# Kernel optimization log

Measured on AMD Instinct MI355X. Metric: run time of the kernel, lower is better.

Reference implementation:

```python
import jax, jax.numpy as jnp
import numpy as np

N = 50000      # nodes
E = 800000     # edges (avg degree 16)
F_IN = 128
H = 128
C = 64


def _lin(k, fan_in, fan_out):
    bound = 1.0 / np.sqrt(fan_in)
    kw, kb = jax.random.split(k)
    W = jax.random.uniform(kw, (fan_in, fan_out), jnp.float32, -bound, bound)
    b = jax.random.uniform(kb, (fan_out,), jnp.float32, -bound, bound)
    return W, b


def setup_inputs() -> dict:
    key = jax.random.key(0)
    ks = jax.random.split(key, 8)
    W1, b1 = _lin(ks[3], F_IN, H)
    W2, b2 = _lin(ks[4], H, H)
    W3, b3 = _lin(ks[5], H, H)
    Wr, br = _lin(ks[6], F_IN, H)
    Wo, bo = _lin(ks[7], H, C)
    return {
        "x": jax.random.normal(ks[0], (N, F_IN), jnp.float32),
        "src": jax.random.randint(ks[1], (E,), 0, N, jnp.int32),
        "dst": jax.random.randint(ks[2], (E,), 0, N, jnp.int32),
        "W1": W1, "b1": b1,
        "W2": W2, "b2": b2,
        "W3": W3, "b3": b3,
        "Wr": Wr, "br": br,
        "Wo": Wo, "bo": bo,
    }


def _degree_norms(src, dst, n):
    ones = jnp.ones(src.shape[0], jnp.float32)
    deg_out = jax.ops.segment_sum(ones, src, num_segments=n)
    deg_in = jax.ops.segment_sum(ones, dst, num_segments=n)
    # DGL norm='both': clamp zero-degree to 1 to avoid inf
    d_src = jnp.where(deg_out > 0, deg_out, 1.0) ** -0.5
    d_dst = jnp.where(deg_in > 0, deg_in, 1.0) ** -0.5
    return d_src, d_dst


def _graph_conv(x, W, b, src, dst, d_src, d_dst, n):
    # h = D_dst^{-1/2} A D_src^{-1/2} (x W) + b
    h = (x * d_src[:, None]) @ W              # [N, out]
    agg = jax.ops.segment_sum(h[src], dst, num_segments=n)  # SpMM via gather/scatter
    return agg * d_dst[:, None] + b


def reference(x, src, dst, W1, b1, W2, b2, W3, b3, Wr, br, Wo, bo):
    n = x.shape[0]
    d_src, d_dst = _degree_norms(src, dst, n)
    res = x @ Wr + br
    out = jax.nn.relu(_graph_conv(x, W1, b1, src, dst, d_src, d_dst, n))
    out = jax.nn.relu(_graph_conv(out, W2, b2, src, dst, d_src, d_dst, n))
    out = _graph_conv(out, W3, b3, src, dst, d_src, d_dst, n)
    out = jax.nn.relu(out + res)
    return out @ Wo + bo
```

## Files before the change

### kernel.cpp

```cpp
#include <hip/hip_runtime.h>
#include <cstdint>
#include <cstddef>

#define FD 128
#define CO 64
#define NB 256
#define NBINS 256

typedef short bf16x8 __attribute__((ext_vector_type(8)));
typedef float f32x4 __attribute__((ext_vector_type(4)));
typedef unsigned int uint32;
typedef unsigned char uint8;

__device__ __forceinline__ unsigned short f2bf(float f) {
  unsigned u = __float_as_uint(f);
  unsigned r = u + 0x7fffu + ((u >> 16) & 1u);
  return (unsigned short)(r >> 16);
}
__device__ __forceinline__ float bf2f(unsigned short b) {
  return __uint_as_float((unsigned)b << 16);
}


__global__ __launch_bounds__(256) void k_hist(const int* __restrict__ src,
                                              const int* __restrict__ dst,
                                              int* __restrict__ histD,
                                              int* __restrict__ histS,
                                              int E, int chunk) {
  __shared__ int hd[NBINS], hs[NBINS];
  int tid = threadIdx.x, blk = blockIdx.x;
  hd[tid] = 0;
  hs[tid] = 0;
  __syncthreads();
  int beg = blk * chunk;
  int end = min(E, beg + chunk);
  for (int e = beg + tid; e < end; e += 256) {
    atomicAdd(&hd[dst[e] >> 8], 1);
    atomicAdd(&hs[src[e] >> 8], 1);
  }
  __syncthreads();
  histD[tid * NB + blk] = hd[tid];
  histS[tid * NB + blk] = hs[tid];
}


__global__ __launch_bounds__(256) void k_ssum(int* __restrict__ a,
                                              int* __restrict__ b,
                                              int* __restrict__ bsums) {
  const int* p = blockIdx.y ? b : a;
  __shared__ int red[256];
  int tid = threadIdx.x;
  red[tid] = p[blockIdx.x * 256 + tid];
  __syncthreads();
  for (int o = 128; o > 0; o >>= 1) {
    if (tid < o) red[tid] += red[tid + o];
    __syncthreads();
  }
  if (tid == 0) bsums[blockIdx.y * 256 + blockIdx.x] = red[0];
}

__global__ __launch_bounds__(256) void k_sscan(int* __restrict__ bsums) {
  __shared__ int s[256];
  int tid = threadIdx.x;
  for (int r = 0; r < 2; r++) {
    int v = bsums[r * 256 + tid];
    s[tid] = v;
    __syncthreads();
    for (int o = 1; o < 256; o <<= 1) {
      int t = (tid >= o) ? s[tid - o] : 0;
      __syncthreads();
      s[tid] += t;
      __syncthreads();
    }
    bsums[r * 256 + tid] = s[tid] - v;
    __syncthreads();
  }
}

__global__ __launch_bounds__(256) void k_sapply(int* __restrict__ a,
                                                int* __restrict__ b,
                                                const int* __restrict__ bsums) {
  int* p = blockIdx.y ? b : a;
  int boff = bsums[blockIdx.y * 256 + blockIdx.x];
  __shared__ int s[256];
  int tid = threadIdx.x;
  int i = blockIdx.x * 256 + tid;
  int v = p[i];
  s[tid] = v;
  __syncthreads();
  for (int o = 1; o < 256; o <<= 1) {
    int t = (tid >= o) ? s[tid - o] : 0;
    __syncthreads();
    s[tid] += t;
    __syncthreads();
  }
  p[i] = boff + s[tid] - v;
}

__global__ __launch_bounds__(256) void k_scatter(const int* __restrict__ src,
                                                 const int* __restrict__ dst,
                                                 const int* __restrict__ offD,
                                                 const int* __restrict__ offS,
                                                 uint32* __restrict__ pk,
                                                 uint8* __restrict__ srcS8,
                                                 int E, int chunk) {
  __shared__ int runD[NBINS], runS[NBINS];
  int tid = threadIdx.x, blk = blockIdx.x;
  runD[tid] = offD[tid * NB + blk];
  runS[tid] = offS[tid * NB + blk];
  __syncthreads();
  int beg = blk * chunk;
  int end = min(E, beg + chunk);
  for (int e = beg + tid; e < end; e += 256) {
    int s = src[e], d = dst[e];
    int p = atomicAdd(&runD[d >> 8], 1);
    pk[p] = ((uint32)s << 8) | (uint32)(d & 255);
    int q = atomicAdd(&runS[s >> 8], 1);
    srcS8[q] = (uint8)(s & 255);
  }
}

__global__ __launch_bounds__(256) void k_bucket_dst(const uint32* __restrict__ pk,
                                                    const int* __restrict__ offD,
                                                    int* __restrict__ esrc,
                                                    int* __restrict__ row_ptr,
                                                    float* __restrict__ d_dst,
                                                    int N, int E) {
  __shared__ int cnt[NBINS], run[NBINS];
  int tid = threadIdx.x, bin = blockIdx.x;
  int start = offD[bin * NB];
  int end = (bin == NBINS - 1) ? E : offD[(bin + 1) * NB];
  cnt[tid] = 0;
  __syncthreads();
  for (int p = start + tid; p < end; p += 256) atomicAdd(&cnt[pk[p] & 255], 1);
  __syncthreads();
  int v = cnt[tid];
  run[tid] = v;
  __syncthreads();
  for (int o = 1; o < 256; o <<= 1) {
    int t = (tid >= o) ? run[tid - o] : 0;
    __syncthreads();
    run[tid] += t;
    __syncthreads();
  }
  int excl = run[tid] - v;
  int node = bin * 256 + tid;
  if (node < N) {
    row_ptr[node] = start + excl;
    d_dst[node] = rsqrtf((float)(v > 0 ? v : 1));
  }
  __syncthreads();
  run[tid] = start + excl;
  __syncthreads();
  for (int p = start + tid; p < end; p += 256) {
    uint32 v2 = pk[p];
    int slot = atomicAdd(&run[v2 & 255], 1);
    esrc[slot] = (int)(v2 >> 8);
  }
  if (bin == 0 && tid == 0) row_ptr[N] = E;
}

__global__ __launch_bounds__(256) void k_bucket_src(const uint8* __restrict__ srcS8,
                                                    const int* __restrict__ offS,
                                                    float* __restrict__ d_src,
                                                    int N, int E) {
  __shared__ int cnt[NBINS];
  int tid = threadIdx.x, bin = blockIdx.x;
  int start = offS[bin * NB];
  int end = (bin == NBINS - 1) ? E : offS[(bin + 1) * NB];
  cnt[tid] = 0;
  __syncthreads();
  for (int p = start + tid; p < end; p += 256) atomicAdd(&cnt[srcS8[p]], 1);
  __syncthreads();
  int node = bin * 256 + tid;
  if (node < N) {
    int v = cnt[tid];
    d_src[node] = rsqrtf((float)(v > 0 ? v : 1));
  }
}


__global__ __launch_bounds__(256) void k_wsplit(const float* __restrict__ W1,
                                                const float* __restrict__ W2,
                                                const float* __restrict__ W3,
                                                const float* __restrict__ Wr,
                                                const float* __restrict__ Wo,
                                                bf16x8* __restrict__ Whg,
                                                bf16x8* __restrict__ Wlg) {
  int idx = blockIdx.x * 256 + threadIdx.x;
  if (idx >= 9216) return;
  int region = idx >> 11;
  if (idx >= 8192) region = 4;
  const float* W = (region == 0) ? W1 : (region == 1) ? W2 : (region == 2) ? W3
                   : (region == 3) ? Wr : Wo;
  int cols = (region < 4) ? FD : CO;
  int local = idx - region * 2048;
  int kc = local / cols, col = local - kc * cols;
  bf16x8 h, l;
#pragma unroll
  for (int j = 0; j < 8; j++) {
    float v = W[(size_t)(kc * 8 + j) * cols + col];
    unsigned short hb = f2bf(v);
    h[j] = (short)hb;
    l[j] = (short)f2bf(v - bf2f(hb));
  }
  Whg[idx] = h;
  Wlg[idx] = l;
}


__global__ __launch_bounds__(256) void k_gemm_dual(const float* __restrict__ x,
                                                   const bf16x8* __restrict__ Wh1,
                                                   const bf16x8* __restrict__ Wl1,
                                                   const float* __restrict__ d_src,
                                                   const bf16x8* __restrict__ Whr,
                                                   const bf16x8* __restrict__ Wlr,
                                                   const float* __restrict__ br,
                                                   unsigned short* __restrict__ out1,
                                                   unsigned short* __restrict__ out2,
                                                   int N) {
  __shared__ bf16x8 Ah[1024];
  int tid = threadIdx.x;
  int rowBase = blockIdx.x * 64;

#pragma unroll
  for (int t = 0; t < 4; t++) {
    int p = t * 256 + tid;
    int kc = p >> 6, row = p & 63;
    int gr = rowBase + row;
    bf16x8 h = {0, 0, 0, 0, 0, 0, 0, 0};
    if (gr < N) {
      const float4* A4 = (const float4*)(x + (size_t)gr * FD + kc * 8);
      float4 u = A4[0];
      float4 v = A4[1];
      float vals[8] = {u.x, u.y, u.z, u.w, v.x, v.y, v.z, v.w};
#pragma unroll
      for (int j = 0; j < 8; j++) h[j] = (short)f2bf(vals[j]);
    }
    Ah[kc * 64 + row] = h;
  }
  __syncthreads();

  int wv = tid >> 6, lane = tid & 63;
  int wr = (wv >> 1) * 32;
  int wc = (wv & 1) * 64;
  int lhi = lane >> 4, llo = lane & 15;

#pragma unroll
  for (int pass = 0; pass < 2; pass++) {
    const bf16x8* Wh = pass ? Whr : Wh1;
    const bf16x8* Wl = pass ? Wlr : Wl1;
    f32x4 acc[2][4] = {};
#pragma unroll
    for (int ks = 0; ks < 4; ks++) {
      int kcg = ks * 4 + lhi;
      int abase = kcg * 64 + wr + llo;
      bf16x8 a0 = Ah[abase];
      bf16x8 a1 = Ah[abase + 16];
      int bbase = kcg * FD + wc + llo;
#pragma unroll
      for (int nf = 0; nf < 4; nf++) {
        bf16x8 bh = Wh[bbase + nf * 16];
        bf16x8 bl = Wl[bbase + nf * 16];
        acc[0][nf] = __builtin_amdgcn_mfma_f32_16x16x32_bf16(a0, bh, acc[0][nf], 0, 0, 0);
        acc[1][nf] = __builtin_amdgcn_mfma_f32_16x16x32_bf16(a1, bh, acc[1][nf], 0, 0, 0);
        acc[0][nf] = __builtin_amdgcn_mfma_f32_16x16x32_bf16(a0, bl, acc[0][nf], 0, 0, 0);
        acc[1][nf] = __builtin_amdgcn_mfma_f32_16x16x32_bf16(a1, bl, acc[1][nf], 0, 0, 0);
      }
    }
#pragma unroll
    for (int nf = 0; nf < 4; nf++) {
      int col = wc + nf * 16 + llo;
      float bv = pass ? br[col] : 0.f;
#pragma unroll
      for (int mf = 0; mf < 2; mf++) {
#pragma unroll
        for (int r = 0; r < 4; r++) {
          int row = rowBase + wr + mf * 16 + lhi * 4 + r;
          if (row < N) {
            float v = acc[mf][nf][r];
            if (pass == 0) v *= d_src[row];
            else v += bv;
            unsigned short* o = pass ? out2 : out1;
            o[(size_t)row * FD + col] = f2bf(v);
          }
        }
      }
    }
  }
}


template <int NCW, bool RES, bool NEXTSCALE, bool BIASOUT, bool OUTBF16>
__global__ __launch_bounds__(512) void k_aggemm(const unsigned short* __restrict__ h,
                                                const int* __restrict__ row_ptr,
                                                const int* __restrict__ esrc,
                                                const float* __restrict__ d_dst,
                                                const float* __restrict__ bias_in,
                                                const float* __restrict__ d_src,
                                                const unsigned short* __restrict__ res,
                                                const bf16x8* __restrict__ Wh,
                                                const bf16x8* __restrict__ Wl,
                                                const float* __restrict__ bias_out,
                                                void* __restrict__ outv, int N) {
  constexpr int NF = NCW / 64;
  __shared__ bf16x8 Alds[1024];
  int tid = threadIdx.x;
  int wv = tid >> 6, lane = tid & 63;
  int rowBase = blockIdx.x * 64;
  int sub = lane >> 4, sl = lane & 15;
  const uint4* h16 = (const uint4*)h;

  float4 bA = ((const float4*)bias_in)[sl * 2];
  float4 bB = ((const float4*)bias_in)[sl * 2 + 1];
  float bia[8] = {bA.x, bA.y, bA.z, bA.w, bB.x, bB.y, bB.z, bB.w};

  for (int rq = 0; rq < 2; rq++) {
    int r = wv * 8 + rq * 4 + sub;
    int gr = rowBase + r;
    float a[8] = {0.f, 0.f, 0.f, 0.f, 0.f, 0.f, 0.f, 0.f};
    float val[8];
    if (gr < N) {
      int beg = row_ptr[gr], end = row_ptr[gr + 1];
      int e = beg;
      for (; e + 8 <= end; e += 8) {
        int s[8];
#pragma unroll
        for (int j = 0; j < 8; j++) s[j] = esrc[e + j];
        uint4 v[8];
#pragma unroll
        for (int j = 0; j < 8; j++) v[j] = h16[(size_t)s[j] * 16 + sl];
#pragma unroll
        for (int j = 0; j < 8; j++) {
          a[0] += bf2f((unsigned short)(v[j].x & 0xffff));
          a[1] += bf2f((unsigned short)(v[j].x >> 16));
          a[2] += bf2f((unsigned short)(v[j].y & 0xffff));
          a[3] += bf2f((unsigned short)(v[j].y >> 16));
          a[4] += bf2f((unsigned short)(v[j].z & 0xffff));
          a[5] += bf2f((unsigned short)(v[j].z >> 16));
          a[6] += bf2f((unsigned short)(v[j].w & 0xffff));
          a[7] += bf2f((unsigned short)(v[j].w >> 16));
        }
      }
      for (; e < end; e++) {
        uint4 v = h16[(size_t)esrc[e] * 16 + sl];
        a[0] += bf2f((unsigned short)(v.x & 0xffff));
        a[1] += bf2f((unsigned short)(v.x >> 16));
        a[2] += bf2f((unsigned short)(v.y & 0xffff));
        a[3] += bf2f((unsigned short)(v.y >> 16));
        a[4] += bf2f((unsigned short)(v.z & 0xffff));
        a[5] += bf2f((unsigned short)(v.z >> 16));
        a[6] += bf2f((unsigned short)(v.w & 0xffff));
        a[7] += bf2f((unsigned short)(v.w >> 16));
      }
      float d = d_dst[gr];
#pragma unroll
      for (int j = 0; j < 8; j++) val[j] = a[j] * d + bia[j];
      if (RES) {
        uint4 rv = ((const uint4*)res)[(size_t)gr * 16 + sl];
        val[0] += bf2f((unsigned short)(rv.x & 0xffff));
        val[1] += bf2f((unsigned short)(rv.x >> 16));
        val[2] += bf2f((unsigned short)(rv.y & 0xffff));
        val[3] += bf2f((unsigned short)(rv.y >> 16));
        val[4] += bf2f((unsigned short)(rv.z & 0xffff));
        val[5] += bf2f((unsigned short)(rv.z >> 16));
        val[6] += bf2f((unsigned short)(rv.w & 0xffff));
        val[7] += bf2f((unsigned short)(rv.w >> 16));
      }
#pragma unroll
      for (int j = 0; j < 8; j++) val[j] = fmaxf(val[j], 0.f);
      if (NEXTSCALE) {
        float sc = d_src[gr];
#pragma unroll
        for (int j = 0; j < 8; j++) val[j] *= sc;
      }
    } else {
#pragma unroll
      for (int j = 0; j < 8; j++) val[j] = 0.f;
    }
    bf16x8 o;
#pragma unroll
    for (int j = 0; j < 8; j++) o[j] = (short)f2bf(val[j]);
    Alds[r * 16 + (sl ^ (r & 7))] = o;
  }
  __syncthreads();

  int wr = (wv >> 2) * 32;
  int wc = (wv & 3) * (NCW / 4);
  int lhi = lane >> 4, llo = lane & 15;
  f32x4 acc[2][NF] = {};

#pragma unroll
  for (int ks = 0; ks < 4; ks++) {
    int kcg = ks * 4 + lhi;
    int row0 = wr + llo;
    int row1 = wr + 16 + llo;
    bf16x8 a0 = Alds[row0 * 16 + (kcg ^ (row0 & 7))];
    bf16x8 a1 = Alds[row1 * 16 + (kcg ^ (row1 & 7))];
    int bbase = kcg * NCW + wc + llo;
#pragma unroll
    for (int nf = 0; nf < NF; nf++) {
      bf16x8 bh = Wh[bbase + nf * 16];
      bf16x8 bl = Wl[bbase + nf * 16];
      acc[0][nf] = __builtin_amdgcn_mfma_f32_16x16x32_bf16(a0, bh, acc[0][nf], 0, 0, 0);
      acc[1][nf] = __builtin_amdgcn_mfma_f32_16x16x32_bf16(a1, bh, acc[1][nf], 0, 0, 0);
      acc[0][nf] = __builtin_amdgcn_mfma_f32_16x16x32_bf16(a0, bl, acc[0][nf], 0, 0, 0);
      acc[1][nf] = __builtin_amdgcn_mfma_f32_16x16x32_bf16(a1, bl, acc[1][nf], 0, 0, 0);
    }
  }

#pragma unroll
  for (int nf = 0; nf < NF; nf++) {
    int col = wc + nf * 16 + llo;
    float bv = BIASOUT ? bias_out[col] : 0.f;
#pragma unroll
    for (int mf = 0; mf < 2; mf++) {
#pragma unroll
      for (int r = 0; r < 4; r++) {
        int row = rowBase + wr + mf * 16 + lhi * 4 + r;
        if (row < N) {
          float v = acc[mf][nf][r] + bv;
          if (OUTBF16)
            ((unsigned short*)outv)[(size_t)row * NCW + col] = f2bf(v);
          else
            ((float*)outv)[(size_t)row * NCW + col] = v;
        }
      }
    }
  }
}


extern "C" void kernel_launch(void* const* d_in, const int* in_sizes, int n_in,
                              void* d_out, int out_size, void* d_ws, size_t ws_size,
                              hipStream_t stream) {
  (void)n_in; (void)out_size; (void)ws_size;
  const float* x  = (const float*)d_in[0];
  const int*   src = (const int*)d_in[1];
  const int*   dst = (const int*)d_in[2];
  const float* W1 = (const float*)d_in[3];
  const float* b1 = (const float*)d_in[4];
  const float* W2 = (const float*)d_in[5];
  const float* b2 = (const float*)d_in[6];
  const float* W3 = (const float*)d_in[7];
  const float* b3 = (const float*)d_in[8];
  const float* Wr = (const float*)d_in[9];
  const float* br = (const float*)d_in[10];
  const float* Wo = (const float*)d_in[11];
  const float* bo = (const float*)d_in[12];
  float* out = (float*)d_out;

  const int N = in_sizes[0] / FD;
  const int E = in_sizes[1];

  char* ws = (char*)d_ws;
  size_t off = 0;
  auto alloc = [&](size_t bytes) -> void* {
    void* p = ws + off;
    off += (bytes + 255) & ~size_t(255);
    return p;
  };
  int* histD   = (int*)alloc((size_t)NBINS * NB * 4);
  int* histS   = (int*)alloc((size_t)NBINS * NB * 4);
  int* bsums   = (int*)alloc(2 * 256 * 4);
  uint32* pk   = (uint32*)alloc((size_t)E * 4);
  uint8* srcS8 = (uint8*)alloc((size_t)E);
  int* esrc    = (int*)alloc((size_t)E * 4);
  int* row_ptr = (int*)alloc((size_t)(N + 1) * 4);
  float* d_src = (float*)alloc((size_t)N * 4);
  float* d_dst = (float*)alloc((size_t)N * 4);
  bf16x8* Whg  = (bf16x8*)alloc(9216 * 16);
  bf16x8* Wlg  = (bf16x8*)alloc(9216 * 16);
  unsigned short* tb0  = (unsigned short*)alloc((size_t)N * FD * 2);
  unsigned short* tb1  = (unsigned short*)alloc((size_t)N * FD * 2);
  unsigned short* resb = (unsigned short*)alloc((size_t)N * FD * 2);

  int chunk = (E + NB - 1) / NB;
  dim3 gScan(256, 2);

  k_wsplit<<<36, 256, 0, stream>>>(W1, W2, W3, Wr, Wo, Whg, Wlg);
  k_hist<<<NB, 256, 0, stream>>>(src, dst, histD, histS, E, chunk);
  k_ssum<<<gScan, 256, 0, stream>>>(histD, histS, bsums);
  k_sscan<<<1, 256, 0, stream>>>(bsums);
  k_sapply<<<gScan, 256, 0, stream>>>(histD, histS, bsums);
  k_scatter<<<NB, 256, 0, stream>>>(src, dst, histD, histS, pk, srcS8, E, chunk);
  k_bucket_dst<<<NBINS, 256, 0, stream>>>(pk, histD, esrc, row_ptr, d_dst, N, E);
  k_bucket_src<<<NBINS, 256, 0, stream>>>(srcS8, histS, d_src, N, E);

  int gG = (N + 63) / 64;

  const bf16x8* Wh1 = Whg;
  const bf16x8* Wh2 = Whg + 2048;
  const bf16x8* Wh3 = Whg + 4096;
  const bf16x8* Whr = Whg + 6144;
  const bf16x8* Who = Whg + 8192;
  const bf16x8* Wl1 = Wlg;
  const bf16x8* Wl2 = Wlg + 2048;
  const bf16x8* Wl3 = Wlg + 4096;
  const bf16x8* Wlr = Wlg + 6144;
  const bf16x8* Wlo = Wlg + 8192;

  k_gemm_dual<<<gG, 256, 0, stream>>>(x, Wh1, Wl1, d_src, Whr, Wlr, br, tb0, resb, N);
  k_aggemm<FD, false, true, false, true><<<gG, 512, 0, stream>>>(
      tb0, row_ptr, esrc, d_dst, b1, d_src, nullptr, Wh2, Wl2, nullptr, tb1, N);
  k_aggemm<FD, false, true, false, true><<<gG, 512, 0, stream>>>(
      tb1, row_ptr, esrc, d_dst, b2, d_src, nullptr, Wh3, Wl3, nullptr, tb0, N);
  k_aggemm<CO, true, false, true, false><<<gG, 512, 0, stream>>>(
      tb0, row_ptr, esrc, d_dst, b3, nullptr, resb, Who, Wlo, bo, out, N);
}
```

Before: 210.0 us.

## Split fused aggregate-GEMM into column-partitioned aggregation and separate GEMM kernels

Replaces the fused aggregation+MFMA kernel with two kernels per layer. The first is a gather aggregation whose grid is split four ways over column quarters, so each thread handles 8 columns for one node. The second is a standalone split-bf16 GEMM that reads the aggregated bf16 intermediate. The aim is more parallelism and better latency hiding for the gather, at the cost of writing and re-reading an extra N×128 bf16 buffer and three more kernel launches. Each edge-index read is also repeated across the four column blocks.

```diff
diff --git a/kernel.cpp b/kernel.cpp
--- a/kernel.cpp
+++ b/kernel.cpp
@@ -11,13 +11,14 @@
 typedef float f32x4 __attribute__((ext_vector_type(4)));
 typedef unsigned int uint32;
 typedef unsigned char uint8;
-
-__device__ __forceinline__ unsigned short f2bf(float f) {
+typedef unsigned short ushort;
+
+__device__ __forceinline__ ushort f2bf(float f) {
   unsigned u = __float_as_uint(f);
   unsigned r = u + 0x7fffu + ((u >> 16) & 1u);
-  return (unsigned short)(r >> 16);
-}
-__device__ __forceinline__ float bf2f(unsigned short b) {
+  return (ushort)(r >> 16);
+}
+__device__ __forceinline__ float bf2f(ushort b) {
   return __uint_as_float((unsigned)b << 16);
 }
 
@@ -42,7 +43,6 @@
   histD[tid * NB + blk] = hd[tid];
   histS[tid * NB + blk] = hs[tid];
 }
-
 
 __global__ __launch_bounds__(256) void k_ssum(int* __restrict__ a,
                                               int* __restrict__ b,
@@ -200,7 +200,7 @@
 #pragma unroll
   for (int j = 0; j < 8; j++) {
     float v = W[(size_t)(kc * 8 + j) * cols + col];
-    unsigned short hb = f2bf(v);
+    ushort hb = f2bf(v);
     h[j] = (short)hb;
     l[j] = (short)f2bf(v - bf2f(hb));
   }
@@ -216,8 +216,8 @@
                                                    const bf16x8* __restrict__ Whr,
                                                    const bf16x8* __restrict__ Wlr,
                                                    const float* __restrict__ br,
-                                                   unsigned short* __restrict__ out1,
-                                                   unsigned short* __restrict__ out2,
+                                                   ushort* __restrict__ out1,
+                                                   ushort* __restrict__ out2,
                                                    int N) {
   __shared__ bf16x8 Ah[1024];
   int tid = threadIdx.x;
@@ -281,7 +281,7 @@
             float v = acc[mf][nf][r];
             if (pass == 0) v *= d_src[row];
             else v += bv;
-            unsigned short* o = pass ? out2 : out1;
+            ushort* o = pass ? out2 : out1;
             o[(size_t)row * FD + col] = f2bf(v);
           }
         }
@@ -291,112 +291,130 @@
 }
 
 
-template <int NCW, bool RES, bool NEXTSCALE, bool BIASOUT, bool OUTBF16>
-__global__ __launch_bounds__(512) void k_aggemm(const unsigned short* __restrict__ h,
-                                                const int* __restrict__ row_ptr,
-                                                const int* __restrict__ esrc,
-                                                const float* __restrict__ d_dst,
-                                                const float* __restrict__ bias_in,
-                                                const float* __restrict__ d_src,
-                                                const unsigned short* __restrict__ res,
-                                                const bf16x8* __restrict__ Wh,
-                                                const bf16x8* __restrict__ Wl,
-                                                const float* __restrict__ bias_out,
-                                                void* __restrict__ outv, int N) {
-  constexpr int NF = NCW / 64;
-  __shared__ bf16x8 Alds[1024];
+template <bool RES, bool NEXTSCALE>
+__global__ __launch_bounds__(256) void k_agg4(const ushort* __restrict__ h,
+                                              const int* __restrict__ row_ptr,
+                                              const int* __restrict__ esrc,
+                                              const float* __restrict__ d_dst,
+                                              const float* __restrict__ bias_in,
+                                              const float* __restrict__ d_src,
+                                              const ushort* __restrict__ res,
+                                              ushort* __restrict__ out,
+                                              int N, int nodeBlocks) {
+  int blk = blockIdx.x;
+  int q = blk / nodeBlocks;
+  int nb = blk - q * nodeBlocks;
   int tid = threadIdx.x;
+  int sub = tid >> 2, sl = tid & 3;
+  int node = nb * 64 + sub;
+  if (node >= N) return;
+  int colSlot = q * 4 + sl;
+  const uint4* h16 = (const uint4*)h;
+
+  float4 bA = ((const float4*)bias_in)[q * 8 + sl * 2];
+  float4 bB = ((const float4*)bias_in)[q * 8 + sl * 2 + 1];
+  float bia[8] = {bA.x, bA.y, bA.z, bA.w, bB.x, bB.y, bB.z, bB.w};
+
+  int beg = row_ptr[node], end = row_ptr[node + 1];
+  float a[8] = {0.f, 0.f, 0.f, 0.f, 0.f, 0.f, 0.f, 0.f};
+  int e = beg;
+  for (; e + 8 <= end; e += 8) {
+    int s[8];
+#pragma unroll
+    for (int j = 0; j < 8; j++) s[j] = esrc[e + j];
+    uint4 v[8];
+#pragma unroll
+    for (int j = 0; j < 8; j++) v[j] = h16[(size_t)s[j] * 16 + colSlot];
+#pragma unroll
+    for (int j = 0; j < 8; j++) {
+      a[0] += bf2f((ushort)(v[j].x & 0xffff));
+      a[1] += bf2f((ushort)(v[j].x >> 16));
+      a[2] += bf2f((ushort)(v[j].y & 0xffff));
+      a[3] += bf2f((ushort)(v[j].y >> 16));
+      a[4] += bf2f((ushort)(v[j].z & 0xffff));
+      a[5] += bf2f((ushort)(v[j].z >> 16));
+      a[6] += bf2f((ushort)(v[j].w & 0xffff));
+      a[7] += bf2f((ushort)(v[j].w >> 16));
+    }
+  }
+  for (; e < end; e++) {
+    uint4 v = h16[(size_t)esrc[e] * 16 + colSlot];
+    a[0] += bf2f((ushort)(v.x & 0xffff));
+    a[1] += bf2f((ushort)(v.x >> 16));
+    a[2] += bf2f((ushort)(v.y & 0xffff));
+    a[3] += bf2f((ushort)(v.y >> 16));
+    a[4] += bf2f((ushort)(v.z & 0xffff));
+    a[5] += bf2f((ushort)(v.z >> 16));
+    a[6] += bf2f((ushort)(v.w & 0xffff));
+    a[7] += bf2f((ushort)(v.w >> 16));
+  }
+
+  float d = d_dst[node];
+  float val[8];
+#pragma unroll
+  for (int j = 0; j < 8; j++) val[j] = a[j] * d + bia[j];
+  if (RES) {
+    uint4 rv = ((const uint4*)res)[(size_t)node * 16 + colSlot];
+    val[0] += bf2f((ushort)(rv.x & 0xffff));
+    val[1] += bf2f((ushort)(rv.x >> 16));
+    val[2] += bf2f((ushort)(rv.y & 0xffff));
+    val[3] += bf2f((ushort)(rv.y >> 16));
+    val[4] += bf2f((ushort)(rv.z & 0xffff));
+    val[5] += bf2f((ushort)(rv.z >> 16));
+    val[6] += bf2f((ushort)(rv.w & 0xffff));
+    val[7] += bf2f((ushort)(rv.w >> 16));
+  }
+#pragma unroll
+  for (int j = 0; j < 8; j++) val[j] = fmaxf(val[j], 0.f);
+  if (NEXTSCALE) {
+    float sc = d_src[node];
+#pragma unroll
+    for (int j = 0; j < 8; j++) val[j] *= sc;
+  }
+  uint32 w0 = (uint32)f2bf(val[0]) | ((uint32)f2bf(val[1]) << 16);
+  uint32 w1 = (uint32)f2bf(val[2]) | ((uint32)f2bf(val[3]) << 16);
+  uint32 w2 = (uint32)f2bf(val[4]) | ((uint32)f2bf(val[5]) << 16);
+  uint32 w3 = (uint32)f2bf(val[6]) | ((uint32)f2bf(val[7]) << 16);
+  uint4 o;
+  o.x = w0; o.y = w1; o.z = w2; o.w = w3;
+  ((uint4*)out)[(size_t)node * 16 + colSlot] = o;
+}
+
+
+template <int NCW, bool BIAS, bool OUTBF16>
+__global__ __launch_bounds__(256) void k_gemmB(const ushort* __restrict__ A,
+                                               const bf16x8* __restrict__ Wh,
+                                               const bf16x8* __restrict__ Wl,
+                                               const float* __restrict__ bias,
+                                               void* __restrict__ outv, int N) {
+  constexpr int NF = NCW / 32;
+  __shared__ bf16x8 Ah[1024];
+  int tid = threadIdx.x;
+  int rowBase = blockIdx.x * 64;
+
+#pragma unroll
+  for (int t = 0; t < 4; t++) {
+    int p = t * 256 + tid;
+    int kc = p >> 6, row = p & 63;
+    int gr = rowBase + row;
+    bf16x8 h = {0, 0, 0, 0, 0, 0, 0, 0};
+    if (gr < N) h = *(const bf16x8*)(A + (size_t)gr * FD + kc * 8);
+    Ah[kc * 64 + row] = h;
+  }
+  __syncthreads();
+
   int wv = tid >> 6, lane = tid & 63;
-  int rowBase = blockIdx.x * 64;
-  int sub = lane >> 4, sl = lane & 15;
-  const uint4* h16 = (const uint4*)h;
-
-  float4 bA = ((const float4*)bias_in)[sl * 2];
-  float4 bB = ((const float4*)bias_in)[sl * 2 + 1];
-  float bia[8] = {bA.x, bA.y, bA.z, bA.w, bB.x, bB.y, bB.z, bB.w};
-
-  for (int rq = 0; rq < 2; rq++) {
-    int r = wv * 8 + rq * 4 + sub;
-    int gr = rowBase + r;
-    float a[8] = {0.f, 0.f, 0.f, 0.f, 0.f, 0.f, 0.f, 0.f};
-    float val[8];
-    if (gr < N) {
-      int beg = row_ptr[gr], end = row_ptr[gr + 1];
-      int e = beg;
-      for (; e + 8 <= end; e += 8) {
-        int s[8];
-#pragma unroll
-        for (int j = 0; j < 8; j++) s[j] = esrc[e + j];
-        uint4 v[8];
-#pragma unroll
-        for (int j = 0; j < 8; j++) v[j] = h16[(size_t)s[j] * 16 + sl];
-#pragma unroll
-        for (int j = 0; j < 8; j++) {
-          a[0] += bf2f((unsigned short)(v[j].x & 0xffff));
-          a[1] += bf2f((unsigned short)(v[j].x >> 16));
-          a[2] += bf2f((unsigned short)(v[j].y & 0xffff));
-          a[3] += bf2f((unsigned short)(v[j].y >> 16));
-          a[4] += bf2f((unsigned short)(v[j].z & 0xffff));
-          a[5] += bf2f((unsigned short)(v[j].z >> 16));
-          a[6] += bf2f((unsigned short)(v[j].w & 0xffff));
-          a[7] += bf2f((unsigned short)(v[j].w >> 16));
-        }
-      }
-      for (; e < end; e++) {
-        uint4 v = h16[(size_t)esrc[e] * 16 + sl];
-        a[0] += bf2f((unsigned short)(v.x & 0xffff));
-        a[1] += bf2f((unsigned short)(v.x >> 16));
-        a[2] += bf2f((unsigned short)(v.y & 0xffff));
-        a[3] += bf2f((unsigned short)(v.y >> 16));
-        a[4] += bf2f((unsigned short)(v.z & 0xffff));
-        a[5] += bf2f((unsigned short)(v.z >> 16));
-        a[6] += bf2f((unsigned short)(v.w & 0xffff));
-        a[7] += bf2f((unsigned short)(v.w >> 16));
-      }
-      float d = d_dst[gr];
-#pragma unroll
-      for (int j = 0; j < 8; j++) val[j] = a[j] * d + bia[j];
-      if (RES) {
-        uint4 rv = ((const uint4*)res)[(size_t)gr * 16 + sl];
-        val[0] += bf2f((unsigned short)(rv.x & 0xffff));
-        val[1] += bf2f((unsigned short)(rv.x >> 16));
-        val[2] += bf2f((unsigned short)(rv.y & 0xffff));
-        val[3] += bf2f((unsigned short)(rv.y >> 16));
-        val[4] += bf2f((unsigned short)(rv.z & 0xffff));
-        val[5] += bf2f((unsigned short)(rv.z >> 16));
-        val[6] += bf2f((unsigned short)(rv.w & 0xffff));
-        val[7] += bf2f((unsigned short)(rv.w >> 16));
-      }
-#pragma unroll
-      for (int j = 0; j < 8; j++) val[j] = fmaxf(val[j], 0.f);
-      if (NEXTSCALE) {
-        float sc = d_src[gr];
-#pragma unroll
-        for (int j = 0; j < 8; j++) val[j] *= sc;
-      }
-    } else {
-#pragma unroll
-      for (int j = 0; j < 8; j++) val[j] = 0.f;
-    }
-    bf16x8 o;
-#pragma unroll
-    for (int j = 0; j < 8; j++) o[j] = (short)f2bf(val[j]);
-    Alds[r * 16 + (sl ^ (r & 7))] = o;
-  }
-  __syncthreads();
-
-  int wr = (wv >> 2) * 32;
-  int wc = (wv & 3) * (NCW / 4);
+  int wr = (wv >> 1) * 32;
+  int wc = (wv & 1) * (NCW / 2);
   int lhi = lane >> 4, llo = lane & 15;
   f32x4 acc[2][NF] = {};
 
 #pragma unroll
   for (int ks = 0; ks < 4; ks++) {
     int kcg = ks * 4 + lhi;
-    int row0 = wr + llo;
-    int row1 = wr + 16 + llo;
-    bf16x8 a0 = Alds[row0 * 16 + (kcg ^ (row0 & 7))];
-    bf16x8 a1 = Alds[row1 * 16 + (kcg ^ (row1 & 7))];
+    int abase = kcg * 64 + wr + llo;
+    bf16x8 a0 = Ah[abase];
+    bf16x8 a1 = Ah[abase + 16];
     int bbase = kcg * NCW + wc + llo;
 #pragma unroll
     for (int nf = 0; nf < NF; nf++) {
@@ -412,7 +430,7 @@
 #pragma unroll
   for (int nf = 0; nf < NF; nf++) {
     int col = wc + nf * 16 + llo;
-    float bv = BIASOUT ? bias_out[col] : 0.f;
+    float bv = BIAS ? bias[col] : 0.f;
 #pragma unroll
     for (int mf = 0; mf < 2; mf++) {
 #pragma unroll
@@ -421,7 +439,7 @@
         if (row < N) {
           float v = acc[mf][nf][r] + bv;
           if (OUTBF16)
-            ((unsigned short*)outv)[(size_t)row * NCW + col] = f2bf(v);
+            ((ushort*)outv)[(size_t)row * NCW + col] = f2bf(v);
           else
             ((float*)outv)[(size_t)row * NCW + col] = v;
         }
@@ -471,9 +489,10 @@
   float* d_dst = (float*)alloc((size_t)N * 4);
   bf16x8* Whg  = (bf16x8*)alloc(9216 * 16);
   bf16x8* Wlg  = (bf16x8*)alloc(9216 * 16);
-  unsigned short* tb0  = (unsigned short*)alloc((size_t)N * FD * 2);
-  unsigned short* tb1  = (unsigned short*)alloc((size_t)N * FD * 2);
-  unsigned short* resb = (unsigned short*)alloc((size_t)N * FD * 2);
+  ushort* tb0  = (ushort*)alloc((size_t)N * FD * 2);
+  ushort* tb1  = (ushort*)alloc((size_t)N * FD * 2);
+  ushort* tba  = (ushort*)alloc((size_t)N * FD * 2);
+  ushort* resb = (ushort*)alloc((size_t)N * FD * 2);
 
   int chunk = (E + NB - 1) / NB;
   dim3 gScan(256, 2);
@@ -488,6 +507,8 @@
   k_bucket_src<<<NBINS, 256, 0, stream>>>(srcS8, histS, d_src, N, E);
 
   int gG = (N + 63) / 64;
+  int nodeBlocks = (N + 63) / 64;
+  int gA = nodeBlocks * 4;
 
   const bf16x8* Wh1 = Whg;
   const bf16x8* Wh2 = Whg + 2048;
@@ -501,10 +522,13 @@
   const bf16x8* Wlo = Wlg + 8192;
 
   k_gemm_dual<<<gG, 256, 0, stream>>>(x, Wh1, Wl1, d_src, Whr, Wlr, br, tb0, resb, N);
-  k_aggemm<FD, false, true, false, true><<<gG, 512, 0, stream>>>(
-      tb0, row_ptr, esrc, d_dst, b1, d_src, nullptr, Wh2, Wl2, nullptr, tb1, N);
-  k_aggemm<FD, false, true, false, true><<<gG, 512, 0, stream>>>(
-      tb1, row_ptr, esrc, d_dst, b2, d_src, nullptr, Wh3, Wl3, nullptr, tb0, N);
-  k_aggemm<CO, true, false, true, false><<<gG, 512, 0, stream>>>(
-      tb0, row_ptr, esrc, d_dst, b3, nullptr, resb, Who, Wlo, bo, out, N);
-}
+  k_agg4<false, true><<<gA, 256, 0, stream>>>(tb0, row_ptr, esrc, d_dst, b1, d_src,
+                                              nullptr, tba, N, nodeBlocks);
+  k_gemmB<FD, false, true><<<gG, 256, 0, stream>>>(tba, Wh2, Wl2, nullptr, tb1, N);
+  k_agg4<false, true><<<gA, 256, 0, stream>>>(tb1, row_ptr, esrc, d_dst, b2, d_src,
+                                              nullptr, tba, N, nodeBlocks);
+  k_gemmB<FD, false, true><<<gG, 256, 0, stream>>>(tba, Wh3, Wl3, nullptr, tb0, N);
+  k_agg4<true, false><<<gA, 256, 0, stream>>>(tb0, row_ptr, esrc, d_dst, b3, nullptr,
+                                              resb, tba, N, nodeBlocks);
+  k_gemmB<CO, true, false><<<gG, 256, 0, stream>>>(tba, Who, Wlo, bo, out, N);
+}
```

Result: slower. 253.4 us (+20.7%).

## Use 16-bit edge indices and 1024-thread aggregation blocks with deeper gather unroll

Applied to the files above, without the earlier changes.

Edge source indices in the CSR are stored as 16-bit values instead of 32-bit, halving index traffic in the gather loops. The aggregate+GEMM kernel now runs 1024 threads per block, so each 16-lane group handles one row instead of two and each wave does a 16-row MFMA tile. The neighbor gather unrolls by 16 with a masked tail instead of 8 plus a scalar tail. The aim is more outstanding memory requests for the latency-bound gather. The 16-bit indices only work while the node count stays below 65536, and the larger blocks may lower occupancy flexibility.

```diff
diff --git a/kernel.cpp b/kernel.cpp
--- a/kernel.cpp
+++ b/kernel.cpp
@@ -11,13 +11,14 @@
 typedef float f32x4 __attribute__((ext_vector_type(4)));
 typedef unsigned int uint32;
 typedef unsigned char uint8;
-
-__device__ __forceinline__ unsigned short f2bf(float f) {
+typedef unsigned short ushort;
+
+__device__ __forceinline__ ushort f2bf(float f) {
   unsigned u = __float_as_uint(f);
   unsigned r = u + 0x7fffu + ((u >> 16) & 1u);
-  return (unsigned short)(r >> 16);
-}
-__device__ __forceinline__ float bf2f(unsigned short b) {
+  return (ushort)(r >> 16);
+}
+__device__ __forceinline__ float bf2f(ushort b) {
   return __uint_as_float((unsigned)b << 16);
 }
 
@@ -42,7 +43,6 @@
   histD[tid * NB + blk] = hd[tid];
   histS[tid * NB + blk] = hs[tid];
 }
-
 
 __global__ __launch_bounds__(256) void k_ssum(int* __restrict__ a,
                                               int* __restrict__ b,
@@ -122,7 +122,7 @@
 
 __global__ __launch_bounds__(256) void k_bucket_dst(const uint32* __restrict__ pk,
                                                     const int* __restrict__ offD,
-                                                    int* __restrict__ esrc,
+                                                    ushort* __restrict__ esrc,
                                                     int* __restrict__ row_ptr,
                                                     float* __restrict__ d_dst,
                                                     int N, int E) {
@@ -155,7 +155,7 @@
   for (int p = start + tid; p < end; p += 256) {
     uint32 v2 = pk[p];
     int slot = atomicAdd(&run[v2 & 255], 1);
-    esrc[slot] = (int)(v2 >> 8);
+    esrc[slot] = (ushort)(v2 >> 8);
   }
   if (bin == 0 && tid == 0) row_ptr[N] = E;
 }
@@ -200,7 +200,7 @@
 #pragma unroll
   for (int j = 0; j < 8; j++) {
     float v = W[(size_t)(kc * 8 + j) * cols + col];
-    unsigned short hb = f2bf(v);
+    ushort hb = f2bf(v);
     h[j] = (short)hb;
     l[j] = (short)f2bf(v - bf2f(hb));
   }
@@ -216,8 +216,8 @@
                                                    const bf16x8* __restrict__ Whr,
                                                    const bf16x8* __restrict__ Wlr,
                                                    const float* __restrict__ br,
-                                                   unsigned short* __restrict__ out1,
-                                                   unsigned short* __restrict__ out2,
+                                                   ushort* __restrict__ out1,
+                                                   ushort* __restrict__ out2,
                                                    int N) {
   __shared__ bf16x8 Ah[1024];
   int tid = threadIdx.x;
@@ -281,7 +281,7 @@
             float v = acc[mf][nf][r];
             if (pass == 0) v *= d_src[row];
             else v += bv;
-            unsigned short* o = pass ? out2 : out1;
+            ushort* o = pass ? out2 : out1;
             o[(size_t)row * FD + col] = f2bf(v);
           }
         }
@@ -292,120 +292,126 @@
 
 
 template <int NCW, bool RES, bool NEXTSCALE, bool BIASOUT, bool OUTBF16>
-__global__ __launch_bounds__(512) void k_aggemm(const unsigned short* __restrict__ h,
-                                                const int* __restrict__ row_ptr,
-                                                const int* __restrict__ esrc,
-                                                const float* __restrict__ d_dst,
-                                                const float* __restrict__ bias_in,
-                                                const float* __restrict__ d_src,
-                                                const unsigned short* __restrict__ res,
-                                                const bf16x8* __restrict__ Wh,
-                                                const bf16x8* __restrict__ Wl,
-                                                const float* __restrict__ bias_out,
-                                                void* __restrict__ outv, int N) {
+__global__ __launch_bounds__(1024) void k_aggemm(const ushort* __restrict__ h,
+                                                 const int* __restrict__ row_ptr,
+                                                 const ushort* __restrict__ esrc,
+                                                 const float* __restrict__ d_dst,
+                                                 const float* __restrict__ bias_in,
+                                                 const float* __restrict__ d_src,
+                                                 const ushort* __restrict__ res,
+                                                 const bf16x8* __restrict__ Wh,
+                                                 const bf16x8* __restrict__ Wl,
+                                                 const float* __restrict__ bias_out,
+                                                 void* __restrict__ outv, int N) {
   constexpr int NF = NCW / 64;
   __shared__ bf16x8 Alds[1024];
   int tid = threadIdx.x;
   int wv = tid >> 6, lane = tid & 63;
   int rowBase = blockIdx.x * 64;
   int sub = lane >> 4, sl = lane & 15;
+  int r = wv * 4 + sub;
+  int gr = rowBase + r;
   const uint4* h16 = (const uint4*)h;
 
   float4 bA = ((const float4*)bias_in)[sl * 2];
   float4 bB = ((const float4*)bias_in)[sl * 2 + 1];
   float bia[8] = {bA.x, bA.y, bA.z, bA.w, bB.x, bB.y, bB.z, bB.w};
 
-  for (int rq = 0; rq < 2; rq++) {
-    int r = wv * 8 + rq * 4 + sub;
-    int gr = rowBase + r;
+  float val[8];
+#pragma unroll
+  for (int j = 0; j < 8; j++) val[j] = 0.f;
+
+  if (gr < N) {
+    int beg = row_ptr[gr], end = row_ptr[gr + 1];
     float a[8] = {0.f, 0.f, 0.f, 0.f, 0.f, 0.f, 0.f, 0.f};
-    float val[8];
-    if (gr < N) {
-      int beg = row_ptr[gr], end = row_ptr[gr + 1];
-      int e = beg;
-      for (; e + 8 <= end; e += 8) {
-        int s[8];
-#pragma unroll
-        for (int j = 0; j < 8; j++) s[j] = esrc[e + j];
-        uint4 v[8];
-#pragma unroll
-        for (int j = 0; j < 8; j++) v[j] = h16[(size_t)s[j] * 16 + sl];
-#pragma unroll
-        for (int j = 0; j < 8; j++) {
-          a[0] += bf2f((unsigned short)(v[j].x & 0xffff));
-          a[1] += bf2f((unsigned short)(v[j].x >> 16));
-          a[2] += bf2f((unsigned short)(v[j].y & 0xffff));
-          a[3] += bf2f((unsigned short)(v[j].y >> 16));
-          a[4] += bf2f((unsigned short)(v[j].z & 0xffff));
-          a[5] += bf2f((unsigned short)(v[j].z >> 16));
-          a[6] += bf2f((unsigned short)(v[j].w & 0xffff));
-          a[7] += bf2f((unsigned short)(v[j].w >> 16));
+    int e = beg;
+    for (; e + 16 <= end; e += 16) {
+      int s[16];
+#pragma unroll
+      for (int j = 0; j < 16; j++) s[j] = esrc[e + j];
+      uint4 v[16];
+#pragma unroll
+      for (int j = 0; j < 16; j++) v[j] = h16[(size_t)s[j] * 16 + sl];
+#pragma unroll
+      for (int j = 0; j < 16; j++) {
+        a[0] += bf2f((ushort)(v[j].x & 0xffff));
+        a[1] += bf2f((ushort)(v[j].x >> 16));
+        a[2] += bf2f((ushort)(v[j].y & 0xffff));
+        a[3] += bf2f((ushort)(v[j].y >> 16));
+        a[4] += bf2f((ushort)(v[j].z & 0xffff));
+        a[5] += bf2f((ushort)(v[j].z >> 16));
+        a[6] += bf2f((ushort)(v[j].w & 0xffff));
+        a[7] += bf2f((ushort)(v[j].w >> 16));
+      }
+    }
+    if (e < end) {
+      int cnt = end - e;
+      int s[16];
+#pragma unroll
+      for (int j = 0; j < 16; j++) s[j] = (j < cnt) ? (int)esrc[e + j] : 0;
+      uint4 v[16];
+#pragma unroll
+      for (int j = 0; j < 16; j++)
+        if (j < cnt) v[j] = h16[(size_t)s[j] * 16 + sl];
+#pragma unroll
+      for (int j = 0; j < 16; j++) {
+        if (j < cnt) {
+          a[0] += bf2f((ushort)(v[j].x & 0xffff));
+          a[1] += bf2f((ushort)(v[j].x >> 16));
+          a[2] += bf2f((ushort)(v[j].y & 0xffff));
+          a[3] += bf2f((ushort)(v[j].y >> 16));
+          a[4] += bf2f((ushort)(v[j].z & 0xffff));
+          a[5] += bf2f((ushort)(v[j].z >> 16));
+          a[6] += bf2f((ushort)(v[j].w & 0xffff));
+          a[7] += bf2f((ushort)(v[j].w >> 16));
         }
       }
-      for (; e < end; e++) {
-        uint4 v = h16[(size_t)esrc[e] * 16 + sl];
-        a[0] += bf2f((unsigned short)(v.x & 0xffff));
-        a[1] += bf2f((unsigned short)(v.x >> 16));
-        a[2] += bf2f((unsigned short)(v.y & 0xffff));
-        a[3] += bf2f((unsigned short)(v.y >> 16));
-        a[4] += bf2f((unsigned short)(v.z & 0xffff));
-        a[5] += bf2f((unsigned short)(v.z >> 16));
-        a[6] += bf2f((unsigned short)(v.w & 0xffff));
-        a[7] += bf2f((unsigned short)(v.w >> 16));
-      }
-      float d = d_dst[gr];
-#pragma unroll
-      for (int j = 0; j < 8; j++) val[j] = a[j] * d + bia[j];
-      if (RES) {
-        uint4 rv = ((const uint4*)res)[(size_t)gr * 16 + sl];
-        val[0] += bf2f((unsigned short)(rv.x & 0xffff));
-        val[1] += bf2f((unsigned short)(rv.x >> 16));
-        val[2] += bf2f((unsigned short)(rv.y & 0xffff));
-        val[3] += bf2f((unsigned short)(rv.y >> 16));
-        val[4] += bf2f((unsigned short)(rv.z & 0xffff));
-        val[5] += bf2f((unsigned short)(rv.z >> 16));
-        val[6] += bf2f((unsigned short)(rv.w & 0xffff));
-        val[7] += bf2f((unsigned short)(rv.w >> 16));
-      }
-#pragma unroll
-      for (int j = 0; j < 8; j++) val[j] = fmaxf(val[j], 0.f);
-      if (NEXTSCALE) {
-        float sc = d_src[gr];
-#pragma unroll
-        for (int j = 0; j < 8; j++) val[j] *= sc;
-      }
-    } else {
-#pragma unroll
-      for (int j = 0; j < 8; j++) val[j] = 0.f;
-    }
-    bf16x8 o;
-#pragma unroll
-    for (int j = 0; j < 8; j++) o[j] = (short)f2bf(val[j]);
-    Alds[r * 16 + (sl ^ (r & 7))] = o;
-  }
-  __syncthreads();
-
-  int wr = (wv >> 2) * 32;
+    }
+    float d = d_dst[gr];
+#pragma unroll
+    for (int j = 0; j < 8; j++) val[j] = a[j] * d + bia[j];
+    if (RES) {
+      uint4 rv = ((const uint4*)res)[(size_t)gr * 16 + sl];
+      val[0] += bf2f((ushort)(rv.x & 0xffff));
+      val[1] += bf2f((ushort)(rv.x >> 16));
+      val[2] += bf2f((ushort)(rv.y & 0xffff));
+      val[3] += bf2f((ushort)(rv.y >> 16));
+      val[4] += bf2f((ushort)(rv.z & 0xffff));
+      val[5] += bf2f((ushort)(rv.z >> 16));
+      val[6] += bf2f((ushort)(rv.w & 0xffff));
+      val[7] += bf2f((ushort)(rv.w >> 16));
+    }
+#pragma unroll
+    for (int j = 0; j < 8; j++) val[j] = fmaxf(val[j], 0.f);
+    if (NEXTSCALE) {
+      float sc = d_src[gr];
+#pragma unroll
+      for (int j = 0; j < 8; j++) val[j] *= sc;
+    }
+  }
+  bf16x8 o;
+#pragma unroll
+  for (int j = 0; j < 8; j++) o[j] = (short)f2bf(val[j]);
+  Alds[r * 16 + (sl ^ (r & 7))] = o;
+  __syncthreads();
+
+  int wr = (wv >> 2) * 16;
   int wc = (wv & 3) * (NCW / 4);
   int lhi = lane >> 4, llo = lane & 15;
-  f32x4 acc[2][NF] = {};
+  f32x4 acc[NF] = {};
 
 #pragma unroll
   for (int ks = 0; ks < 4; ks++) {
     int kcg = ks * 4 + lhi;
     int row0 = wr + llo;
-    int row1 = wr + 16 + llo;
     bf16x8 a0 = Alds[row0 * 16 + (kcg ^ (row0 & 7))];
-    bf16x8 a1 = Alds[row1 * 16 + (kcg ^ (row1 & 7))];
     int bbase = kcg * NCW + wc + llo;
 #pragma unroll
     for (int nf = 0; nf < NF; nf++) {
       bf16x8 bh = Wh[bbase + nf * 16];
       bf16x8 bl = Wl[bbase + nf * 16];
-      acc[0][nf] = __builtin_amdgcn_mfma_f32_16x16x32_bf16(a0, bh, acc[0][nf], 0, 0, 0);
-      acc[1][nf] = __builtin_amdgcn_mfma_f32_16x16x32_bf16(a1, bh, acc[1][nf], 0, 0, 0);
-      acc[0][nf] = __builtin_amdgcn_mfma_f32_16x16x32_bf16(a0, bl, acc[0][nf], 0, 0, 0);
-      acc[1][nf] = __builtin_amdgcn_mfma_f32_16x16x32_bf16(a1, bl, acc[1][nf], 0, 0, 0);
+      acc[nf] = __builtin_amdgcn_mfma_f32_16x16x32_bf16(a0, bh, acc[nf], 0, 0, 0);
+      acc[nf] = __builtin_amdgcn_mfma_f32_16x16x32_bf16(a0, bl, acc[nf], 0, 0, 0);
     }
   }
 
@@ -414,17 +420,14 @@
     int col = wc + nf * 16 + llo;
     float bv = BIASOUT ? bias_out[col] : 0.f;
 #pragma unroll
-    for (int mf = 0; mf < 2; mf++) {
-#pragma unroll
-      for (int r = 0; r < 4; r++) {
-        int row = rowBase + wr + mf * 16 + lhi * 4 + r;
-        if (row < N) {
-          float v = acc[mf][nf][r] + bv;
-          if (OUTBF16)
-            ((unsigned short*)outv)[(size_t)row * NCW + col] = f2bf(v);
-          else
-            ((float*)outv)[(size_t)row * NCW + col] = v;
-        }
+    for (int rr = 0; rr < 4; rr++) {
+      int row = rowBase + wr + lhi * 4 + rr;
+      if (row < N) {
+        float v = acc[nf][rr] + bv;
+        if (OUTBF16)
+          ((ushort*)outv)[(size_t)row * NCW + col] = f2bf(v);
+        else
+          ((float*)outv)[(size_t)row * NCW + col] = v;
       }
     }
   }
@@ -465,15 +468,15 @@
   int* bsums   = (int*)alloc(2 * 256 * 4);
   uint32* pk   = (uint32*)alloc((size_t)E * 4);
   uint8* srcS8 = (uint8*)alloc((size_t)E);
-  int* esrc    = (int*)alloc((size_t)E * 4);
+  ushort* esrc = (ushort*)alloc((size_t)E * 2);
   int* row_ptr = (int*)alloc((size_t)(N + 1) * 4);
   float* d_src = (float*)alloc((size_t)N * 4);
   float* d_dst = (float*)alloc((size_t)N * 4);
   bf16x8* Whg  = (bf16x8*)alloc(9216 * 16);
   bf16x8* Wlg  = (bf16x8*)alloc(9216 * 16);
-  unsigned short* tb0  = (unsigned short*)alloc((size_t)N * FD * 2);
-  unsigned short* tb1  = (unsigned short*)alloc((size_t)N * FD * 2);
-  unsigned short* resb = (unsigned short*)alloc((size_t)N * FD * 2);
+  ushort* tb0  = (ushort*)alloc((size_t)N * FD * 2);
+  ushort* tb1  = (ushort*)alloc((size_t)N * FD * 2);
+  ushort* resb = (ushort*)alloc((size_t)N * FD * 2);
 
   int chunk = (E + NB - 1) / NB;
   dim3 gScan(256, 2);
@@ -501,10 +504,10 @@
   const bf16x8* Wlo = Wlg + 8192;
 
   k_gemm_dual<<<gG, 256, 0, stream>>>(x, Wh1, Wl1, d_src, Whr, Wlr, br, tb0, resb, N);
-  k_aggemm<FD, false, true, false, true><<<gG, 512, 0, stream>>>(
+  k_aggemm<FD, false, true, false, true><<<gG, 1024, 0, stream>>>(
       tb0, row_ptr, esrc, d_dst, b1, d_src, nullptr, Wh2, Wl2, nullptr, tb1, N);
-  k_aggemm<FD, false, true, false, true><<<gG, 512, 0, stream>>>(
+  k_aggemm<FD, false, true, false, true><<<gG, 1024, 0, stream>>>(
       tb1, row_ptr, esrc, d_dst, b2, d_src, nullptr, Wh3, Wl3, nullptr, tb0, N);
-  k_aggemm<CO, true, false, true, false><<<gG, 512, 0, stream>>>(
+  k_aggemm<CO, true, false, true, false><<<gG, 1024, 0, stream>>>(
       tb0, row_ptr, esrc, d_dst, b3, nullptr, resb, Who, Wlo, bo, out, N);
 }
```

Result: slower. 221.2 us (+5.3%).
